# Performance work log

Measured on AMD Instinct MI355X. Metric: run time of the kernel, lower is better.

Reference implementation:

```python
import jax, jax.numpy as jnp
import numpy as np

B, T, D = 2, 2048, 1024
H, HD = 16, 64  # num_heads, key_size

def setup_inputs() -> dict:
    key = jax.random.key(0)
    ks = jax.random.split(key, 5)
    s = 1.0 / np.sqrt(D)  # VarianceScaling(1.0, fan_in) approx
    return {
        "query": jax.random.normal(ks[0], (B, T, D), dtype=jnp.float32),
        "wq": jax.random.normal(ks[1], (D, H * HD), dtype=jnp.float32) * s,
        "bq": jnp.zeros((H * HD,), dtype=jnp.float32),
        "wk": jax.random.normal(ks[2], (D, H * HD), dtype=jnp.float32) * s,
        "bk": jnp.zeros((H * HD,), dtype=jnp.float32),
        "wv": jax.random.normal(ks[3], (D, H * HD), dtype=jnp.float32) * s,
        "bv": jnp.zeros((H * HD,), dtype=jnp.float32),
        "wo": jax.random.normal(ks[4], (H * HD, D), dtype=jnp.float32) * (1.0 / np.sqrt(H * HD)),
        "bo": jnp.zeros((D,), dtype=jnp.float32),
    }

def reference(query, wq, bq, wk, bk, wv, bv, wo, bo):
    b, t, _ = query.shape
    proj = lambda w, bias: (query @ w + bias).reshape(b, t, H, HD)
    q = proj(wq, bq) / np.sqrt(HD).astype(np.float32)  # fixed scaling on queries
    k = proj(wk, bk)
    v = proj(wv, bv)
    logits = jnp.einsum('bthd,bThd->bhtT', q, k)  # [B,H,T,T]
    causal = jnp.tril(jnp.ones((t, t), dtype=logits.dtype))
    logits = logits - 1e10 * (1.0 - causal)
    weights = jax.nn.softmax(logits, axis=-1)
    attn = jnp.einsum('bhtT,bThd->bthd', weights, v)
    attn_vec = attn.reshape(b, t, H * HD)
    return attn_vec @ wo + bo
```

## Files before the change

### kernel.cpp

```cpp
#include <hip/hip_runtime.h>
#include <hip/hip_bf16.h>
#include <stdint.h>
#include <math.h>

typedef short bf16x8 __attribute__((ext_vector_type(8)));
typedef float f32x4 __attribute__((ext_vector_type(4)));
typedef unsigned u32x4v __attribute__((ext_vector_type(4)));
typedef __hip_bfloat16 bf16;

#define MFMA16(a, b, c) __builtin_amdgcn_mfma_f32_16x16x32_bf16((a), (b), (c), 0, 0, 0)

__device__ __forceinline__ void glds16(const void* g, void* l) {
  __builtin_amdgcn_global_load_lds((const __attribute__((address_space(1))) void*)g,
                                   (__attribute__((address_space(3))) void*)l, 16, 0, 0);
}

__device__ __forceinline__ bf16x8 ld8(const bf16* p) {
  return *reinterpret_cast<const bf16x8*>(p);
}

__device__ __forceinline__ void pl32swap(unsigned& a, unsigned& b) {
  asm volatile("v_permlane32_swap_b32 %0, %1" : "+v"(a), "+v"(b));
}
__device__ __forceinline__ void pl16swap(unsigned& a, unsigned& b) {
  asm volatile("v_permlane16_swap_b32 %0, %1" : "+v"(a), "+v"(b));
}


__global__ void k_prep(const float* __restrict__ query,
                       const float* __restrict__ wq, const float* __restrict__ wk,
                       const float* __restrict__ wv, const float* __restrict__ wo,
                       bf16* __restrict__ X, bf16* __restrict__ Wqkvt, bf16* __restrict__ Wot) {
  __shared__ float tile[32][33];
  const int z = blockIdx.z;
  if (z < 4) {
    const float* src = (z == 0) ? wq : (z == 1) ? wk : (z == 2) ? wv : wo;
    bf16* dst = (z < 3) ? (Wqkvt + (size_t)z * 1024 * 1024) : Wot;
    const int tx = threadIdx.x & 31, ty = threadIdx.x >> 5;
    const int x = blockIdx.x * 32 + tx;
    const int y0 = blockIdx.y * 32;
#pragma unroll
    for (int i = 0; i < 4; ++i) tile[ty + i * 8][tx] = src[(size_t)(y0 + ty + i * 8) * 1024 + x];
    __syncthreads();
    const int txh = threadIdx.x & 15, tyh = threadIdx.x >> 4;
#pragma unroll
    for (int i = 0; i < 2; ++i) {
      const int cl = tyh + i * 16;
      const int c = blockIdx.x * 32 + cl;
      bf16 v0 = __float2bfloat16(tile[2 * txh][cl]);
      bf16 v1 = __float2bfloat16(tile[2 * txh + 1][cl]);
      ushort2 pk;
      pk.x = reinterpret_cast<unsigned short&>(v0);
      pk.y = reinterpret_cast<unsigned short&>(v1);
      *reinterpret_cast<ushort2*>(dst + (size_t)c * 1024 + y0 + 2 * txh) = pk;
    }
  } else {
    const int vb = (z - 4) * 1024 + blockIdx.y * 32 + blockIdx.x;
    const int i = vb * 256 + threadIdx.x;
    float4 v = reinterpret_cast<const float4*>(query)[i];
    bf16 a0 = __float2bfloat16(v.x), a1 = __float2bfloat16(v.y);
    bf16 a2 = __float2bfloat16(v.z), a3 = __float2bfloat16(v.w);
    ushort4 r;
    r.x = reinterpret_cast<unsigned short&>(a0);
    r.y = reinterpret_cast<unsigned short&>(a1);
    r.z = reinterpret_cast<unsigned short&>(a2);
    r.w = reinterpret_cast<unsigned short&>(a3);
    reinterpret_cast<ushort4*>(X)[i] = r;
  }
}


__device__ __forceinline__ void gemm_core(const bf16* __restrict__ A, const bf16* __restrict__ Bt,
                                          int K, int arow0, int bcol0,
                                          bf16* As, bf16* Bs, f32x4 acc[4][4]) {
  const int tid = threadIdx.x, lane = tid & 63, w = tid >> 6;
  const int rsub = lane >> 3, slot = lane & 7;
  const int srcslot = slot ^ rsub;
  const int wrow = (w >> 1) * 64, wcol = (w & 1) * 64;
  const int lr = lane & 15, lg = lane >> 4;
  const int nkt = K >> 6;
  for (int kt = 0; kt < nkt; ++kt) {
    const int k0 = kt * 64;
    if (kt) __syncthreads();
#pragma unroll
    for (int i = 0; i < 4; ++i) {
      const int chunk = w * 4 + i;
      glds16(A + (size_t)(arow0 + chunk * 8 + rsub) * K + k0 + srcslot * 8, As + chunk * 512);
      glds16(Bt + (size_t)(bcol0 + chunk * 8 + rsub) * K + k0 + srcslot * 8, Bs + chunk * 512);
    }
    __syncthreads();
#pragma unroll
    for (int kk = 0; kk < 2; ++kk) {
      bf16x8 af[4], bfv[4];
#pragma unroll
      for (int m = 0; m < 4; ++m) {
        const int row = wrow + m * 16 + lr;
        const int byte = (row * 128 + ((kk * 32 + lg * 8) << 1)) ^ ((row & 7) << 4);
        af[m] = *reinterpret_cast<const bf16x8*>(reinterpret_cast<const char*>(As) + byte);
      }
#pragma unroll
      for (int n = 0; n < 4; ++n) {
        const int row = wcol + n * 16 + lr;
        const int byte = (row * 128 + ((kk * 32 + lg * 8) << 1)) ^ ((row & 7) << 4);
        bfv[n] = *reinterpret_cast<const bf16x8*>(reinterpret_cast<const char*>(Bs) + byte);
      }
#pragma unroll
      for (int m = 0; m < 4; ++m)
#pragma unroll
        for (int n = 0; n < 4; ++n) acc[m][n] = MFMA16(af[m], bfv[n], acc[m][n]);
    }
  }
}


__global__ __launch_bounds__(256) void k_gemm_qkv(
    const bf16* __restrict__ X, const bf16* __restrict__ Wt,
    const float* __restrict__ bq, const float* __restrict__ bk, const float* __restrict__ bv,
    bf16* __restrict__ Qo, bf16* __restrict__ Ko, bf16* __restrict__ Vt) {
  __shared__ bf16 As[128 * 64], Bs[128 * 64];
  f32x4 acc[4][4];
#pragma unroll
  for (int i = 0; i < 4; ++i)
#pragma unroll
    for (int j = 0; j < 4; ++j) acc[i][j] = (f32x4){0.f, 0.f, 0.f, 0.f};
  const int orig = blockIdx.x + 24 * blockIdx.y;
  const int xcd = orig & 7, wrem = orig >> 3;
  const int bx = (xcd & 1) * 12 + (wrem % 12);
  const int by = (xcd >> 1) * 8 + (wrem / 12);
  const int arow0 = by * 128, bcol0 = bx * 128;
  gemm_core(X, Wt, 1024, arow0, bcol0, As, Bs, acc);
  const int lane = threadIdx.x & 63, w = threadIdx.x >> 6;
  const int wrow = (w >> 1) * 64, wcol = (w & 1) * 64;
  const int lr = lane & 15, lg = lane >> 4;
  const float QSCALE = 0.125f * 1.4426950408889634f;
#pragma unroll
  for (int mi = 0; mi < 4; ++mi) {
#pragma unroll
    for (int ni = 0; ni < 4; ++ni) {
      const int r0 = arow0 + wrow + mi * 16 + lg * 4;
      const int col = bcol0 + wcol + ni * 16 + lr;
      const int which = col >> 10, cw = col & 1023, h = cw >> 6, hd = cw & 63;
      const int b = r0 >> 11, t0 = r0 & 2047;
      if (which == 2) {
        const float bias = bv[cw];
        ushort4 pk;
#pragma unroll
        for (int j = 0; j < 4; ++j) {
          bf16 hv = __float2bfloat16(acc[mi][ni][j] + bias);
          reinterpret_cast<unsigned short*>(&pk)[j] = reinterpret_cast<unsigned short&>(hv);
        }
        *reinterpret_cast<ushort4*>(Vt + ((size_t)((b * 16 + h) * 64 + hd)) * 2048 + t0) = pk;
      } else {
        const float bias = which ? bk[cw] : bq[cw];
        const float scale = which ? 1.0f : QSCALE;
        bf16* dst = which ? Ko : Qo;
#pragma unroll
        for (int j = 0; j < 4; ++j) {
          float v = (acc[mi][ni][j] + bias) * scale;
          dst[((size_t)((b * 16 + h) * 2048) + t0 + j) * 64 + hd] = __float2bfloat16(v);
        }
      }
    }
  }
}


__global__ __launch_bounds__(256) void k_attn(const bf16* __restrict__ Q, const bf16* __restrict__ Kc,
                                              const bf16* __restrict__ Vt, bf16* __restrict__ attn) {
  __shared__ bf16 Ks[2][64 * 64];
  __shared__ bf16 Vs[2][64 * 64];
  const int lane = threadIdx.x & 63, w = threadIdx.x >> 6;
  const int lr = lane & 15, lg = lane >> 4;
  const int rsub = lane >> 3, slot = lane & 7;
  const int srcslot = slot ^ rsub;
  const int bh = blockIdx.x;
  const int qt = 31 - blockIdx.y;
  const int b = bh >> 4, h = bh & 15;
  const bf16* Qp = Q + (size_t)bh * 2048 * 64;
  const bf16* Kp = Kc + (size_t)bh * 2048 * 64;
  const bf16* Vp = Vt + (size_t)bh * 64 * 2048;

  const int q0 = qt * 64 + w * 16;
  const bf16x8 qa0 = ld8(Qp + (size_t)(q0 + lr) * 64 + lg * 8);
  const bf16x8 qa1 = ld8(Qp + (size_t)(q0 + lr) * 64 + 32 + lg * 8);
  f32x4 o[4], ol;
#pragma unroll
  for (int n = 0; n < 4; ++n) o[n] = (f32x4){0.f, 0.f, 0.f, 0.f};
  ol = (f32x4){0.f, 0.f, 0.f, 0.f};
  const int nkv = qt + 1;
  const float MBIAS = -8.0f * 1.4426950408889634f;
  const f32x4 minit = {MBIAS, MBIAS, MBIAS, MBIAS};
  const short one_bf = (short)0x3F80;
  const bf16x8 ones = {one_bf, one_bf, one_bf, one_bf, one_bf, one_bf, one_bf, one_bf};

#pragma unroll
  for (int i = 0; i < 2; ++i) {
    const int ck = w * 2 + i;
    glds16(Kp + (size_t)(ck * 8 + rsub) * 64 + srcslot * 8, &Ks[0][ck * 512]);
    glds16(Vp + (size_t)(ck * 8 + rsub) * 2048 + srcslot * 8, &Vs[0][ck * 512]);
  }
  __syncthreads();
  int cur = 0;

#pragma unroll 1
  for (int it = 0; it < nkv; ++it) {
    if (it + 1 < nkv) {
#pragma unroll
      for (int i = 0; i < 2; ++i) {
        const int ck = w * 2 + i;
        glds16(Kp + (size_t)((it + 1) * 64 + ck * 8 + rsub) * 64 + srcslot * 8, &Ks[cur ^ 1][ck * 512]);
        glds16(Vp + (size_t)(ck * 8 + rsub) * 2048 + (it + 1) * 64 + srcslot * 8, &Vs[cur ^ 1][ck * 512]);
      }
    }
    f32x4 s[4];
    const char* Kb = reinterpret_cast<const char*>(&Ks[cur][0]);
#pragma unroll
    for (int n = 0; n < 4; ++n) {
      const int row = n * 16 + lr;
      const int rsw = (row & 7) << 4;
      bf16x8 kb0 = *reinterpret_cast<const bf16x8*>(Kb + ((row * 128 + lg * 16) ^ rsw));
      bf16x8 kb1 = *reinterpret_cast<const bf16x8*>(Kb + ((row * 128 + 64 + lg * 16) ^ rsw));
      s[n] = MFMA16(kb0, qa0, minit);
      s[n] = MFMA16(kb1, qa1, s[n]);
    }
    if (it == nkv - 1) {
      const int qme = q0 + lr - it * 64 - lg * 4;
#pragma unroll
      for (int n = 0; n < 4; ++n)
#pragma unroll
        for (int j = 0; j < 4; ++j)
          if (n * 16 + j > qme) s[n][j] = -1e30f;
    }
    float p[4][4];
#pragma unroll
    for (int n = 0; n < 4; ++n)
#pragma unroll
      for (int j = 0; j < 4; ++j) p[n][j] = __builtin_amdgcn_exp2f(s[n][j]);
    unsigned pw[4][2];
#pragma unroll
    for (int n = 0; n < 4; ++n) {
      pw[n][0] = __builtin_amdgcn_perm(__float_as_uint(p[n][1]), __float_as_uint(p[n][0]), 0x07060302u);
      pw[n][1] = __builtin_amdgcn_perm(__float_as_uint(p[n][3]), __float_as_uint(p[n][2]), 0x07060302u);
    }
#pragma unroll
    for (int n1 = 0; n1 < 2; ++n1)
#pragma unroll
      for (int hh = 0; hh < 2; ++hh) {
        pl32swap(pw[2 * n1][hh], pw[2 * n1 + 1][hh]);
        pl16swap(pw[2 * n1][hh], pw[2 * n1 + 1][hh]);
      }
    bf16x8 pa[2];
#pragma unroll
    for (int n1 = 0; n1 < 2; ++n1) {
      u32x4v tv = (u32x4v){pw[2 * n1][0], pw[2 * n1][1], pw[2 * n1 + 1][0], pw[2 * n1 + 1][1]};
      pa[n1] = __builtin_bit_cast(bf16x8, tv);
    }
    ol = MFMA16(pa[0], ones, ol);
    ol = MFMA16(pa[1], ones, ol);
    const char* Vb = reinterpret_cast<const char*>(&Vs[cur][0]);
#pragma unroll
    for (int n2 = 0; n2 < 4; ++n2) {
#pragma unroll
      for (int kc = 0; kc < 2; ++kc) {
        const int row = n2 * 16 + lr;
        const int rsw = (row & 7) << 4;
        bf16x8 vb = *reinterpret_cast<const bf16x8*>(Vb + ((row * 128 + (kc * 32 + lg * 8) * 2) ^ rsw));
        o[n2] = MFMA16(pa[kc], vb, o[n2]);
      }
    }
    __syncthreads();
    cur ^= 1;
  }
#pragma unroll
  for (int j = 0; j < 4; ++j) {
    const float inv = 1.0f / ol[j];
    const int qq = q0 + lg * 4 + j;
#pragma unroll
    for (int n2 = 0; n2 < 4; ++n2)
      attn[((size_t)(b * 2048 + qq)) * 1024 + h * 64 + n2 * 16 + lr] = __float2bfloat16(o[n2][j] * inv);
  }
}


__global__ __launch_bounds__(256) void k_gemm_out(const bf16* __restrict__ A, const bf16* __restrict__ Wot,
                                                  const float* __restrict__ bo, float* __restrict__ out) {
  __shared__ bf16 As[64 * 64], Bs[128 * 64];
  f32x4 acc[4][2];
#pragma unroll
  for (int i = 0; i < 4; ++i)
#pragma unroll
    for (int j = 0; j < 2; ++j) acc[i][j] = (f32x4){0.f, 0.f, 0.f, 0.f};
  const int orig = blockIdx.x + 8 * blockIdx.y;
  const int xcd = orig & 7, wrem = orig >> 3;
  const int bx = (xcd & 1) * 4 + (wrem & 3);
  const int by = (xcd >> 1) * 16 + (wrem >> 2);
  const int arow0 = by * 64, bcol0 = bx * 128;
  const int lane = threadIdx.x & 63, w = threadIdx.x >> 6;
  const int rsub = lane >> 3, slot = lane & 7;
  const int srcslot = slot ^ rsub;
  const int lr = lane & 15, lg = lane >> 4;
  for (int kt = 0; kt < 16; ++kt) {
    const int k0 = kt * 64;
    if (kt) __syncthreads();
#pragma unroll
    for (int i = 0; i < 2; ++i) {
      const int chunk = w * 2 + i;
      glds16(A + (size_t)(arow0 + chunk * 8 + rsub) * 1024 + k0 + srcslot * 8, As + chunk * 512);
    }
#pragma unroll
    for (int i = 0; i < 4; ++i) {
      const int chunk = w * 4 + i;
      glds16(Wot + (size_t)(bcol0 + chunk * 8 + rsub) * 1024 + k0 + srcslot * 8, Bs + chunk * 512);
    }
    __syncthreads();
#pragma unroll
    for (int kk = 0; kk < 2; ++kk) {
      bf16x8 af[4], bfv[2];
#pragma unroll
      for (int m = 0; m < 4; ++m) {
        const int row = m * 16 + lr;
        const int byte = (row * 128 + ((kk * 32 + lg * 8) << 1)) ^ ((row & 7) << 4);
        af[m] = *reinterpret_cast<const bf16x8*>(reinterpret_cast<const char*>(As) + byte);
      }
#pragma unroll
      for (int n = 0; n < 2; ++n) {
        const int row = w * 32 + n * 16 + lr;
        const int byte = (row * 128 + ((kk * 32 + lg * 8) << 1)) ^ ((row & 7) << 4);
        bfv[n] = *reinterpret_cast<const bf16x8*>(reinterpret_cast<const char*>(Bs) + byte);
      }
#pragma unroll
      for (int m = 0; m < 4; ++m)
#pragma unroll
        for (int n = 0; n < 2; ++n) acc[m][n] = MFMA16(af[m], bfv[n], acc[m][n]);
    }
  }
#pragma unroll
  for (int mi = 0; mi < 4; ++mi) {
#pragma unroll
    for (int ni = 0; ni < 2; ++ni) {
      const int r0 = arow0 + mi * 16 + lg * 4;
      const int col = bcol0 + w * 32 + ni * 16 + lr;
      const float bias = bo[col];
#pragma unroll
      for (int j = 0; j < 4; ++j) out[(size_t)(r0 + j) * 1024 + col] = acc[mi][ni][j] + bias;
    }
  }
}


extern "C" void kernel_launch(void* const* d_in, const int* in_sizes, int n_in,
                              void* d_out, int out_size, void* d_ws, size_t ws_size,
                              hipStream_t stream) {
  const float* query = (const float*)d_in[0];
  const float* wq = (const float*)d_in[1];
  const float* bq = (const float*)d_in[2];
  const float* wk = (const float*)d_in[3];
  const float* bk = (const float*)d_in[4];
  const float* wv = (const float*)d_in[5];
  const float* bv = (const float*)d_in[6];
  const float* wo = (const float*)d_in[7];
  const float* bo = (const float*)d_in[8];
  float* out = (float*)d_out;
  char* ws = (char*)d_ws;
  const size_t MB = 1u << 20;
  bf16* X     = (bf16*)(ws + 0);
  bf16* Wqkvt = (bf16*)(ws + 8 * MB);
  bf16* Wot   = (bf16*)(ws + 14 * MB);
  bf16* Qb    = (bf16*)(ws + 16 * MB);
  bf16* Kb    = (bf16*)(ws + 24 * MB);
  bf16* Vt    = (bf16*)(ws + 32 * MB);
  bf16* attn  = (bf16*)(ws + 40 * MB);

  k_prep<<<dim3(32, 32, 8), 256, 0, stream>>>(query, wq, wk, wv, wo, X, Wqkvt, Wot);
  k_gemm_qkv<<<dim3(24, 32), 256, 0, stream>>>(X, Wqkvt, bq, bk, bv, Qb, Kb, Vt);
  k_attn<<<dim3(32, 32), 256, 0, stream>>>(Qb, Kb, Vt, attn);
  k_gemm_out<<<dim3(8, 64), 256, 0, stream>>>(attn, Wot, bo, out);
}
```

Measured before the change: 94.44 us.

## Split attention KV tile across wave pairs with 32-row query fragments and LDS reduction

```diff
diff --git a/kernel.cpp b/kernel.cpp
--- a/kernel.cpp
+++ b/kernel.cpp
@@ -173,6 +173,7 @@
   const int lr = lane & 15, lg = lane >> 4;
   const int rsub = lane >> 3, slot = lane & 7;
   const int srcslot = slot ^ rsub;
+  const int p_ = w >> 1, m_ = w & 1;
   const int bh = blockIdx.x;
   const int qt = 31 - blockIdx.y;
   const int b = bh >> 4, h = bh & 15;
@@ -180,13 +181,20 @@
   const bf16* Kp = Kc + (size_t)bh * 2048 * 64;
   const bf16* Vp = Vt + (size_t)bh * 64 * 2048;
 
-  const int q0 = qt * 64 + w * 16;
-  const bf16x8 qa0 = ld8(Qp + (size_t)(q0 + lr) * 64 + lg * 8);
-  const bf16x8 qa1 = ld8(Qp + (size_t)(q0 + lr) * 64 + 32 + lg * 8);
-  f32x4 o[4], ol;
-#pragma unroll
-  for (int n = 0; n < 4; ++n) o[n] = (f32x4){0.f, 0.f, 0.f, 0.f};
-  ol = (f32x4){0.f, 0.f, 0.f, 0.f};
+  const int qw0 = qt * 64 + m_ * 32;
+  bf16x8 qa[2][2];
+#pragma unroll
+  for (int mf = 0; mf < 2; ++mf) {
+    qa[mf][0] = ld8(Qp + (size_t)(qw0 + mf * 16 + lr) * 64 + lg * 8);
+    qa[mf][1] = ld8(Qp + (size_t)(qw0 + mf * 16 + lr) * 64 + 32 + lg * 8);
+  }
+  f32x4 o[2][4], ol[2];
+#pragma unroll
+  for (int mf = 0; mf < 2; ++mf) {
+    ol[mf] = (f32x4){0.f, 0.f, 0.f, 0.f};
+#pragma unroll
+    for (int n = 0; n < 4; ++n) o[mf][n] = (f32x4){0.f, 0.f, 0.f, 0.f};
+  }
   const int nkv = qt + 1;
   const float MBIAS = -8.0f * 1.4426950408889634f;
   const f32x4 minit = {MBIAS, MBIAS, MBIAS, MBIAS};
@@ -212,72 +220,105 @@
         glds16(Vp + (size_t)(ck * 8 + rsub) * 2048 + (it + 1) * 64 + srcslot * 8, &Vs[cur ^ 1][ck * 512]);
       }
     }
-    f32x4 s[4];
+    bf16x8 kb0[2], kb1[2];
     const char* Kb = reinterpret_cast<const char*>(&Ks[cur][0]);
 #pragma unroll
-    for (int n = 0; n < 4; ++n) {
-      const int row = n * 16 + lr;
+    for (int n_ = 0; n_ < 2; ++n_) {
+      const int row = (2 * p_ + n_) * 16 + lr;
       const int rsw = (row & 7) << 4;
-      bf16x8 kb0 = *reinterpret_cast<const bf16x8*>(Kb + ((row * 128 + lg * 16) ^ rsw));
-      bf16x8 kb1 = *reinterpret_cast<const bf16x8*>(Kb + ((row * 128 + 64 + lg * 16) ^ rsw));
-      s[n] = MFMA16(kb0, qa0, minit);
-      s[n] = MFMA16(kb1, qa1, s[n]);
-    }
+      kb0[n_] = *reinterpret_cast<const bf16x8*>(Kb + ((row * 128 + lg * 16) ^ rsw));
+      kb1[n_] = *reinterpret_cast<const bf16x8*>(Kb + ((row * 128 + 64 + lg * 16) ^ rsw));
+    }
+    f32x4 s[2][2];
+#pragma unroll
+    for (int mf = 0; mf < 2; ++mf)
+#pragma unroll
+      for (int n_ = 0; n_ < 2; ++n_) {
+        s[mf][n_] = MFMA16(kb0[n_], qa[mf][0], minit);
+        s[mf][n_] = MFMA16(kb1[n_], qa[mf][1], s[mf][n_]);
+      }
     if (it == nkv - 1) {
-      const int qme = q0 + lr - it * 64 - lg * 4;
-#pragma unroll
-      for (int n = 0; n < 4; ++n)
-#pragma unroll
-        for (int j = 0; j < 4; ++j)
-          if (n * 16 + j > qme) s[n][j] = -1e30f;
-    }
-    float p[4][4];
-#pragma unroll
-    for (int n = 0; n < 4; ++n)
-#pragma unroll
-      for (int j = 0; j < 4; ++j) p[n][j] = __builtin_amdgcn_exp2f(s[n][j]);
-    unsigned pw[4][2];
-#pragma unroll
-    for (int n = 0; n < 4; ++n) {
-      pw[n][0] = __builtin_amdgcn_perm(__float_as_uint(p[n][1]), __float_as_uint(p[n][0]), 0x07060302u);
-      pw[n][1] = __builtin_amdgcn_perm(__float_as_uint(p[n][3]), __float_as_uint(p[n][2]), 0x07060302u);
-    }
-#pragma unroll
-    for (int n1 = 0; n1 < 2; ++n1)
+#pragma unroll
+      for (int mf = 0; mf < 2; ++mf)
+#pragma unroll
+        for (int n_ = 0; n_ < 2; ++n_) {
+          const int qme = m_ * 32 + mf * 16 + lr - p_ * 32 - lg * 4;
+#pragma unroll
+          for (int j = 0; j < 4; ++j)
+            if (n_ * 16 + j > qme) s[mf][n_][j] = -1e30f;
+        }
+    }
+    float p[2][2][4];
+#pragma unroll
+    for (int mf = 0; mf < 2; ++mf)
+#pragma unroll
+      for (int n_ = 0; n_ < 2; ++n_)
+#pragma unroll
+        for (int j = 0; j < 4; ++j) p[mf][n_][j] = __builtin_amdgcn_exp2f(s[mf][n_][j]);
+    unsigned pw[2][2][2];
+#pragma unroll
+    for (int mf = 0; mf < 2; ++mf)
+#pragma unroll
+      for (int n_ = 0; n_ < 2; ++n_) {
+        pw[mf][n_][0] = __builtin_amdgcn_perm(__float_as_uint(p[mf][n_][1]), __float_as_uint(p[mf][n_][0]), 0x07060302u);
+        pw[mf][n_][1] = __builtin_amdgcn_perm(__float_as_uint(p[mf][n_][3]), __float_as_uint(p[mf][n_][2]), 0x07060302u);
+      }
+    bf16x8 pa[2];
+#pragma unroll
+    for (int mf = 0; mf < 2; ++mf) {
 #pragma unroll
       for (int hh = 0; hh < 2; ++hh) {
-        pl32swap(pw[2 * n1][hh], pw[2 * n1 + 1][hh]);
-        pl16swap(pw[2 * n1][hh], pw[2 * n1 + 1][hh]);
-      }
-    bf16x8 pa[2];
-#pragma unroll
-    for (int n1 = 0; n1 < 2; ++n1) {
-      u32x4v tv = (u32x4v){pw[2 * n1][0], pw[2 * n1][1], pw[2 * n1 + 1][0], pw[2 * n1 + 1][1]};
-      pa[n1] = __builtin_bit_cast(bf16x8, tv);
-    }
-    ol = MFMA16(pa[0], ones, ol);
-    ol = MFMA16(pa[1], ones, ol);
+        pl32swap(pw[mf][0][hh], pw[mf][1][hh]);
+        pl16swap(pw[mf][0][hh], pw[mf][1][hh]);
+      }
+      u32x4v tv = (u32x4v){pw[mf][0][0], pw[mf][0][1], pw[mf][1][0], pw[mf][1][1]};
+      pa[mf] = __builtin_bit_cast(bf16x8, tv);
+    }
+#pragma unroll
+    for (int mf = 0; mf < 2; ++mf) ol[mf] = MFMA16(pa[mf], ones, ol[mf]);
     const char* Vb = reinterpret_cast<const char*>(&Vs[cur][0]);
 #pragma unroll
     for (int n2 = 0; n2 < 4; ++n2) {
-#pragma unroll
-      for (int kc = 0; kc < 2; ++kc) {
-        const int row = n2 * 16 + lr;
-        const int rsw = (row & 7) << 4;
-        bf16x8 vb = *reinterpret_cast<const bf16x8*>(Vb + ((row * 128 + (kc * 32 + lg * 8) * 2) ^ rsw));
-        o[n2] = MFMA16(pa[kc], vb, o[n2]);
-      }
+      const int row = n2 * 16 + lr;
+      const int rsw = (row & 7) << 4;
+      bf16x8 vb = *reinterpret_cast<const bf16x8*>(Vb + ((row * 128 + (p_ * 32 + lg * 8) * 2) ^ rsw));
+#pragma unroll
+      for (int mf = 0; mf < 2; ++mf) o[mf][n2] = MFMA16(pa[mf], vb, o[mf][n2]);
     }
     __syncthreads();
     cur ^= 1;
   }
-#pragma unroll
-  for (int j = 0; j < 4; ++j) {
-    const float inv = 1.0f / ol[j];
-    const int qq = q0 + lg * 4 + j;
-#pragma unroll
-    for (int n2 = 0; n2 < 4; ++n2)
-      attn[((size_t)(b * 2048 + qq)) * 1024 + h * 64 + n2 * 16 + lr] = __float2bfloat16(o[n2][j] * inv);
+
+  f32x4* redo = reinterpret_cast<f32x4*>(&Ks[0][0]);
+  f32x4* redl = reinterpret_cast<f32x4*>(&Vs[0][0]);
+  if (p_ == 1) {
+#pragma unroll
+    for (int mf = 0; mf < 2; ++mf) {
+#pragma unroll
+      for (int n2 = 0; n2 < 4; ++n2) redo[m_ * 512 + (mf * 4 + n2) * 64 + lane] = o[mf][n2];
+      redl[m_ * 128 + mf * 64 + lane] = ol[mf];
+    }
+  }
+  __syncthreads();
+  if (p_ == 0) {
+#pragma unroll
+    for (int mf = 0; mf < 2; ++mf) {
+#pragma unroll
+      for (int n2 = 0; n2 < 4; ++n2) o[mf][n2] += redo[m_ * 512 + (mf * 4 + n2) * 64 + lane];
+      ol[mf] += redl[m_ * 128 + mf * 64 + lane];
+    }
+#pragma unroll
+    for (int mf = 0; mf < 2; ++mf) {
+#pragma unroll
+      for (int j = 0; j < 4; ++j) {
+        const float inv = 1.0f / ol[mf][j];
+        const int qq = qw0 + mf * 16 + lg * 4 + j;
+#pragma unroll
+        for (int n2 = 0; n2 < 4; ++n2)
+          attn[((size_t)(b * 2048 + qq)) * 1024 + h * 64 + n2 * 16 + lr] =
+              __float2bfloat16(o[mf][n2][j] * inv);
+      }
+    }
   }
 }
 
```

Result: faster. 92.08 us (-2.5%).
